# Performance work log

Measured on AMD Instinct MI355X. Metric: run time of the kernel, lower is better.

## Reference

```python
import jax, jax.numpy as jnp
import numpy as np

VOCAB = 2          # len(CHAR_VOCAB) in source
CE = 16            # char_embed_dim
CNN_OUT = 32 + 64 + 128  # 224
EMBED = 64


def _conv1d(x, w, b, pad):
    # x: [N, Cin, L]; w: [Cout, Cin, K]; torch Conv1d semantics
    y = jax.lax.conv_general_dilated(
        x, w, window_strides=(1,), padding=[(pad, pad)],
        dimension_numbers=('NCH', 'OIH', 'NCH'))
    return y + b[None, :, None]


def setup_inputs() -> dict:
    key = jax.random.key(0)
    ks = jax.random.split(key, 12)
    B, S, MC = 32, 2048, 20
    char_ids = jax.random.randint(ks[0], (B, S, MC), 0, VOCAB, dtype=jnp.int64)
    E = jax.random.normal(ks[1], (VOCAB, CE), jnp.float32)
    E = E.at[0].set(0.0)  # padding_idx=0
    s = 0.05
    return {
        'char_ids': char_ids,
        'E': E,
        'W1': jax.random.normal(ks[2], (32, CE, 1), jnp.float32) * s,
        'b1': jnp.zeros((32,), jnp.float32),
        'W2': jax.random.normal(ks[3], (64, CE, 2), jnp.float32) * s,
        'b2': jnp.zeros((64,), jnp.float32),
        'W3': jax.random.normal(ks[4], (128, CE, 3), jnp.float32) * s,
        'b3': jnp.zeros((128,), jnp.float32),
        'Ht_W': jax.random.normal(ks[5], (CNN_OUT, CNN_OUT), jnp.float32) * s,
        'Ht_b': jnp.zeros((CNN_OUT,), jnp.float32),
        'Hg_W': jax.random.normal(ks[6], (CNN_OUT, CNN_OUT), jnp.float32) * s,
        'Hg_b': jnp.zeros((CNN_OUT,), jnp.float32),
        'P_W': jax.random.normal(ks[7], (EMBED, CNN_OUT), jnp.float32) * s,
        'P_b': jnp.zeros((EMBED,), jnp.float32),
    }


def reference(char_ids, E, W1, b1, W2, b2, W3, b3, Ht_W, Ht_b, Hg_W, Hg_b, P_W, P_b):
    B, S, MC = char_ids.shape
    ids = char_ids.reshape(-1, MC)                      # [N, MC]
    emb = E[ids]                                        # [N, MC, CE]
    x = jnp.transpose(emb, (0, 2, 1))                   # [N, CE, MC]
    p1 = jnp.max(jax.nn.relu(_conv1d(x, W1, b1, 0)), axis=2)  # [N, 32]
    p2 = jnp.max(jax.nn.relu(_conv1d(x, W2, b2, 1)), axis=2)  # [N, 64]
    p3 = jnp.max(jax.nn.relu(_conv1d(x, W3, b3, 1)), axis=2)  # [N, 128]
    cnn = jnp.concatenate([p1, p2, p3], axis=1)         # [N, 224]
    t = jax.nn.relu(cnn @ Ht_W.T + Ht_b)
    g = jax.nn.sigmoid(cnn @ Hg_W.T + Hg_b)
    hw = g * t + (1.0 - g) * cnn
    out = hw @ P_W.T + P_b                              # [N, 64]
    return out.reshape(B, S, -1)
```

## Files before the change

### kernel.cpp

```cpp
#include <hip/hip_runtime.h>


typedef _Float16 f16;
typedef __attribute__((ext_vector_type(8))) _Float16 f16x8;
typedef __attribute__((ext_vector_type(4))) float f32x4;

#define LC1   0
#define LRAW2 96
#define LT2   672
#define LRAW3 1696
#define LT3LO 5152
#define LT3HI 7200
#define WOFFB    18944
#define PBASE    100352
#define NWTH     114688
#define UOUT_OFF 278528
#define NKEYS    4096
#define CROW     232
#define LUT_BLOCKS 45
#define REPACK_BLOCKS 448

__device__ __forceinline__ f16x8 hmax8(f16x8 a, f16x8 b) {
  return __builtin_elementwise_max(a, b);
}

__device__ __forceinline__ f16x8 pin8(f16x8 v) {
  union { f16x8 v; unsigned w[4]; } x; x.v = v;
  asm volatile("" : "+v"(x.w[0]), "+v"(x.w[1]), "+v"(x.w[2]), "+v"(x.w[3]) :: "memory");
  return x.v;
}

__device__ __forceinline__ float xs(const float* __restrict__ E, int s, int i) {
  return (s == 0) ? 0.f : E[(s - 1) * 16 + i];
}

__global__ __launch_bounds__(256) void prep_kernel(
    const float* __restrict__ E,
    const float* __restrict__ W1, const float* __restrict__ b1,
    const float* __restrict__ W2, const float* __restrict__ b2,
    const float* __restrict__ W3, const float* __restrict__ b3,
    const float* __restrict__ HtW, const float* __restrict__ HgW,
    const float* __restrict__ PW,
    f16* __restrict__ tab, f16* __restrict__ wsb)
{
  const int tid = threadIdx.x;
  const int bid = blockIdx.x;

  if (bid >= LUT_BLOCKS) {
    int idx = (bid - LUT_BLOCKS) * 256 + tid;
    if (idx < NWTH) {
      int e, isG = 0, isP = 0;
      if (idx < 50176)        { e = idx; }
      else if (idx < 100352)  { e = idx - 50176; isG = 1; }
      else                    { e = idx - 100352; isP = 1; }
      int col = e / 224, k = e - col * 224;
      int nf = col >> 4, kf = k >> 5, kr = k & 31;
      int lane = (col & 15) + ((kr >> 3) << 4), j = kr & 7;
      if (!isP) {
        int off = nf * 7168 + (isG * 7 + kf) * 512 + lane * 8 + j;
        wsb[off] = (f16)(isG ? HgW[e] : HtW[e]);
      } else {
        float w = PW[e];
        f16 hi = (f16)w;
        int off = PBASE + nf * 7168 + kf * 512 + lane * 8 + j;
        wsb[off] = hi;
        wsb[off + 3584] = (f16)(w - (float)hi);
      }
    }
    return;
  }

  if (bid < 27) {
    if (tid >= 128) return;
    const int c = tid, p = bid;
    const int sa = p / 9, sb = (p / 3) % 3, sc = p % 3;
    const float* w = W3 + c * 48;
    float acc = b3[c];
#pragma unroll
    for (int i = 0; i < 16; i++)
      acc += w[i * 3 + 0] * xs(E, sa, i) + w[i * 3 + 1] * xs(E, sb, i)
           + w[i * 3 + 2] * xs(E, sc, i);
    tab[LRAW3 + p * 128 + c] = (f16)acc;
    return;
  }
  if (bid < 43) {
    if (tid >= 128) return;
    const int c = tid, s = bid - 27;
    const float* w = W3 + c * 48;
    float lo = -65504.f, hi = -65504.f;
#pragma unroll
    for (int b = 0; b < 4; b++) {
      if (!((s >> b) & 1)) continue;
      int pl = 13 + 3 * (b >> 1) + (b & 1);
      int ph = 22 + 3 * (b >> 1) + (b & 1);
      int sal = pl / 9, sbl = (pl / 3) % 3, scl = pl % 3;
      int sah = ph / 9, sbh = (ph / 3) % 3, sch = ph % 3;
      float al = b3[c], ah = b3[c];
#pragma unroll
      for (int i = 0; i < 16; i++) {
        al += w[i * 3 + 0] * xs(E, sal, i) + w[i * 3 + 1] * xs(E, sbl, i)
            + w[i * 3 + 2] * xs(E, scl, i);
        ah += w[i * 3 + 0] * xs(E, sah, i) + w[i * 3 + 1] * xs(E, sbh, i)
            + w[i * 3 + 2] * xs(E, sch, i);
      }
      lo = fmaxf(lo, al);
      hi = fmaxf(hi, ah);
    }
    tab[LT3LO + s * 128 + c] = (f16)lo;
    tab[LT3HI + s * 128 + c] = (f16)hi;
    return;
  }
  if (bid == 43) {
    const int c = tid & 63, part = tid >> 6;
    const float* w = W2 + c * 32;
    if (part < 2) {
      int p0 = part * 5;
      int pend = part ? 9 : 5;
      for (int p = p0; p < pend; p++) {
        int sa = p / 3, sb = p % 3;
        float acc = b2[c];
#pragma unroll
        for (int i = 0; i < 16; i++)
          acc += w[i * 2 + 0] * xs(E, sa, i) + w[i * 2 + 1] * xs(E, sb, i);
        tab[LRAW2 + p * 64 + c] = (f16)acc;
      }
    } else {
      float u[4];
#pragma unroll
      for (int b = 0; b < 4; b++) {
        int p = 4 + 3 * (b >> 1) + (b & 1);
        int sa = p / 3, sb = p % 3;
        float acc = b2[c];
#pragma unroll
        for (int i = 0; i < 16; i++)
          acc += w[i * 2 + 0] * xs(E, sa, i) + w[i * 2 + 1] * xs(E, sb, i);
        u[b] = acc;
      }
      int s0 = (part - 2) * 8;
#pragma unroll
      for (int j = 0; j < 8; j++) {
        int s = s0 + j;
        float m = -65504.f;
#pragma unroll
        for (int b = 0; b < 4; b++)
          if ((s >> b) & 1) m = fmaxf(m, u[b]);
        tab[LT2 + s * 64 + c] = (f16)m;
      }
    }
    return;
  }
  {
    if (tid >= 32) return;
    const int c = tid;
    const float* w = W1 + c * 16;
    float u1 = b1[c], u2 = b1[c];
#pragma unroll
    for (int i = 0; i < 16; i++) {
      u1 += w[i] * E[i];
      u2 += w[i] * E[16 + i];
    }
    tab[LC1 + 0 * 32 + c] = (f16)fmaxf(u1, u2);
    tab[LC1 + 1 * 32 + c] = (f16)u1;
    tab[LC1 + 2 * 32 + c] = (f16)u2;
  }
}

__global__ __launch_bounds__(256) void ucompute_kernel(
    const f16* __restrict__ tab, const f16* __restrict__ wsb,
    const float* __restrict__ Htb, const float* __restrict__ Hgb,
    const float* __restrict__ Pb, float* __restrict__ uout)
{
  __shared__ __attribute__((aligned(16))) f16 cnn[16 * CROW];

  const int tid = threadIdx.x;
  const int wave = tid >> 6, lane = tid & 63;
  const int kbase = blockIdx.x * 16;
  const int lrow = lane & 15;
  const int kg8 = (lane >> 4) * 8;
  const int rr0 = (lane >> 4) * 4;

  const int p1row = tid >> 4;
  const int p1g = tid & 15;
  unsigned mw, mb;
  {
    unsigned key = (unsigned)(kbase + p1row);
    unsigned m3i = key & 255u;
    int st1 = 1 + (int)((key >> 8) & 1),  st2 = 1 + (int)((key >> 9) & 1);
    int st19 = 1 + (int)((key >> 10) & 1), st20 = 1 + (int)((key >> 11) & 1);
    unsigned m2i = 0, mchar = 0;
#pragma unroll
    for (int p = 0; p < 8; p++)
      if ((m3i >> p) & 1) {
        m2i |= (1u << (p >> 1)) | (1u << (p & 3));
        mchar |= (1u << ((p >> 2) & 1)) | (1u << ((p >> 1) & 1)) | (1u << (p & 1));
      }
    unsigned sel = (mchar == 3u) ? 0u : ((mchar & 1u) ? 1u : 2u);
    mw = m3i | (m2i << 8) | (sel << 12);
    mb = (unsigned)st1 | ((unsigned)(st20 * 3) << 4)
       | ((unsigned)(st1 * 3 + st2) << 8) | ((unsigned)(st19 * 9 + st20 * 3) << 16);
  }

  const f16x8 KZ = {0, 0, 0, 0, 0, 0, 0, 0};
  {
    const int m3 = mw & 255;
    f16x8 v = hmax8(*(const f16x8*)(tab + LT3LO + (m3 & 15) * 128 + p1g * 8),
                    *(const f16x8*)(tab + LT3HI + ((m3 >> 4) & 15) * 128 + p1g * 8));
    v = hmax8(v, *(const f16x8*)(tab + LRAW3 + ((mb >> 8) & 15) * 128 + p1g * 8));
    v = hmax8(v, *(const f16x8*)(tab + LRAW3 + ((mb >> 16) & 31) * 128 + p1g * 8));
    *(f16x8*)&cnn[p1row * CROW + 96 + p1g * 8] = hmax8(v, KZ);
    if (p1g < 8) {
      f16x8 u = *(const f16x8*)(tab + LT2 + ((mw >> 8) & 15) * 64 + p1g * 8);
      u = hmax8(u, *(const f16x8*)(tab + LRAW2 + (mb & 15) * 64 + p1g * 8));
      u = hmax8(u, *(const f16x8*)(tab + LRAW2 + ((mb >> 4) & 15) * 64 + p1g * 8));
      *(f16x8*)&cnn[p1row * CROW + 32 + p1g * 8] = hmax8(u, KZ);
    }
    if (p1g < 4) {
      int sel = (mw >> 12) & 3;
      f16x8 w = *(const f16x8*)(tab + LC1 + sel * 32 + p1g * 8);
      *(f16x8*)&cnn[p1row * CROW + p1g * 8] = hmax8(w, KZ);
    }
  }
  __syncthreads();

  f16x8 af[7];
#pragma unroll
  for (int kf = 0; kf < 7; kf++)
    af[kf] = *(const f16x8*)&cnn[lrow * CROW + kf * 32 + kg8];
#pragma unroll
  for (int kf = 0; kf < 7; kf++) af[kf] = pin8(af[kf]);
  __syncthreads();

  const f16* wbase = wsb + lane * 8;
  const int nf_cnt = (wave < 2) ? 4 : 3;
  for (int i = 0; i < nf_cnt; i++) {
    const int nf = wave + i * 4;
    const int col = nf * 16 + lrow;
    const f16* p_ = wbase + nf * 7168;
    const float bt = Htb[col], bg = Hgb[col];
    f32x4 aT = {bt, bt, bt, bt};
    f32x4 aG = {bg, bg, bg, bg};
#pragma unroll
    for (int kf = 0; kf < 7; kf++) {
      f16x8 wTv = *(const f16x8*)(p_ + kf * 512);
      f16x8 wGv = *(const f16x8*)(p_ + 3584 + kf * 512);
      aT = __builtin_amdgcn_mfma_f32_16x16x32_f16(af[kf], wTv, aT, 0, 0, 0);
      aG = __builtin_amdgcn_mfma_f32_16x16x32_f16(af[kf], wGv, aG, 0, 0, 0);
    }
#pragma unroll
    for (int r = 0; r < 4; r++) {
      int row = rr0 + r;
      float t  = fmaxf(aT[r], 0.f);
      float gg = __builtin_amdgcn_rcpf(1.f + __expf(-aG[r]));
      float cv = (float)cnn[row * CROW + col];
      cnn[row * CROW + col] = (f16)(cv + gg * (t - cv));
    }
  }
  __syncthreads();

  f16x8 ah[7];
#pragma unroll
  for (int kf = 0; kf < 7; kf++)
    ah[kf] = *(const f16x8*)&cnn[lrow * CROW + kf * 32 + kg8];
  {
    const int col = wave * 16 + lrow;
    const float bp = Pb[col];
    f32x4 ac = {bp, bp, bp, bp};
    const f16* ph = wbase + PBASE + wave * 7168;
#pragma unroll
    for (int kf = 0; kf < 7; kf++) {
      f16x8 wh = *(const f16x8*)(ph + kf * 512);
      f16x8 wl = *(const f16x8*)(ph + 3584 + kf * 512);
      ac = __builtin_amdgcn_mfma_f32_16x16x32_f16(ah[kf], wh, ac, 0, 0, 0);
      ac = __builtin_amdgcn_mfma_f32_16x16x32_f16(ah[kf], wl, ac, 0, 0, 0);
    }
#pragma unroll
    for (int r = 0; r < 4; r++)
      uout[(size_t)(kbase + rr0 + r) * 64 + col] = ac[r];
  }
}

__global__ __launch_bounds__(256) void keyscatter_kernel(
    const int* __restrict__ ids, const float* __restrict__ uout,
    float* __restrict__ out, int n_tok)
{
  __shared__ unsigned keys[64];
  const int tid = threadIdx.x;
  const int tok0 = blockIdx.x * 64;

  if (tid < 64) {
    unsigned key = 0;
    int t = tok0 + tid;
    if (t < n_tok) {
      const int4* idp4 = (const int4*)(ids + (size_t)t * 20);
      int st[21];
#pragma unroll
      for (int q = 0; q < 5; q++) {
        int4 v = idp4[q];
        st[q * 4 + 1] = v.x; st[q * 4 + 2] = v.y;
        st[q * 4 + 3] = v.z; st[q * 4 + 4] = v.w;
      }
      unsigned m3i = 0;
#pragma unroll
      for (int l = 1; l <= 18; l++)
        m3i |= 1u << ((st[l] << 2) | (st[l + 1] << 1) | st[l + 2]);
      key = m3i | ((unsigned)st[1] << 8) | ((unsigned)st[2] << 9)
          | ((unsigned)st[19] << 10) | ((unsigned)st[20] << 11);
    }
    keys[tid] = key;
  }
  __syncthreads();

  const int tl = tid >> 2, q = tid & 3;
  const int t = tok0 + tl;
  if (t >= n_tok) return;
  const f32x4* src = (const f32x4*)(uout + (size_t)keys[tl] * 64 + q * 16);
  f32x4 v0 = src[0], v1 = src[1], v2 = src[2], v3 = src[3];
  f32x4* dst = (f32x4*)(out + (size_t)t * 64 + q * 16);
  dst[0] = v0; dst[1] = v1; dst[2] = v2; dst[3] = v3;
}

extern "C" void kernel_launch(void* const* d_in, const int* in_sizes, int n_in,
                              void* d_out, int out_size, void* d_ws, size_t ws_size,
                              hipStream_t stream) {
  const int*   ids = (const int*)d_in[0];
  const float* E   = (const float*)d_in[1];
  const float* W1  = (const float*)d_in[2];
  const float* b1  = (const float*)d_in[3];
  const float* W2  = (const float*)d_in[4];
  const float* b2  = (const float*)d_in[5];
  const float* W3  = (const float*)d_in[6];
  const float* b3  = (const float*)d_in[7];
  const float* HtW = (const float*)d_in[8];
  const float* Htb = (const float*)d_in[9];
  const float* HgW = (const float*)d_in[10];
  const float* Hgb = (const float*)d_in[11];
  const float* PW  = (const float*)d_in[12];
  const float* Pb  = (const float*)d_in[13];
  float* out = (float*)d_out;
  char* ws = (char*)d_ws;
  f16* tab = (f16*)ws;
  f16* wsb = (f16*)(ws + WOFFB);
  float* uout = (float*)(ws + UOUT_OFF);
  const int n_tok = in_sizes[0] / 20;

  prep_kernel<<<LUT_BLOCKS + REPACK_BLOCKS, 256, 0, stream>>>(
      E, W1, b1, W2, b2, W3, b3, HtW, HgW, PW, tab, wsb);
  ucompute_kernel<<<NKEYS / 16, 256, 0, stream>>>(
      tab, wsb, Htb, Hgb, Pb, uout);
  keyscatter_kernel<<<(n_tok + 63) / 64, 256, 0, stream>>>(ids, uout, out, n_tok);
}
```

Baseline: 28.29 us.

## Move per-token key computation into prep kernel and widen scatter blocks

Per-token key hashing of the char ids moves out of the final scatter kernel into extra blocks of the prep kernel, so reading the large id array overlaps with weight repacking and LUT building instead of sitting on the critical path before the gather. The scatter kernel now reads precomputed 4-byte keys and handles 256 tokens per block across four segments, launching fewer blocks. This adds a workspace array of keys and an extra global write and read of those keys, and it makes the prep launch larger.

```diff
diff --git a/kernel.cpp b/kernel.cpp
--- a/kernel.cpp
+++ b/kernel.cpp
@@ -14,11 +14,13 @@
 #define WOFFB    18944
 #define PBASE    100352
 #define NWTH     114688
-#define UOUT_OFF 278528
+#define TKEY_OFF 278528
+#define UOUT_OFF 544768
 #define NKEYS    4096
 #define CROW     232
 #define LUT_BLOCKS 45
 #define REPACK_BLOCKS 448
+#define KEY_BLOCKS 256
 
 __device__ __forceinline__ f16x8 hmax8(f16x8 a, f16x8 b) {
   return __builtin_elementwise_max(a, b);
@@ -40,11 +42,32 @@
     const float* __restrict__ W2, const float* __restrict__ b2,
     const float* __restrict__ W3, const float* __restrict__ b3,
     const float* __restrict__ HtW, const float* __restrict__ HgW,
-    const float* __restrict__ PW,
-    f16* __restrict__ tab, f16* __restrict__ wsb)
+    const float* __restrict__ PW, const int* __restrict__ ids,
+    f16* __restrict__ tab, f16* __restrict__ wsb,
+    unsigned* __restrict__ tokkey, int n_tok)
 {
   const int tid = threadIdx.x;
   const int bid = blockIdx.x;
+
+  if (bid >= LUT_BLOCKS + REPACK_BLOCKS) {
+    int t = (bid - LUT_BLOCKS - REPACK_BLOCKS) * 256 + tid;
+    if (t >= n_tok) return;
+    const int4* idp4 = (const int4*)(ids + (size_t)t * 20);
+    int st[21];
+#pragma unroll
+    for (int q = 0; q < 5; q++) {
+      int4 v = idp4[q];
+      st[q * 4 + 1] = v.x; st[q * 4 + 2] = v.y;
+      st[q * 4 + 3] = v.z; st[q * 4 + 4] = v.w;
+    }
+    unsigned m3i = 0;
+#pragma unroll
+    for (int l = 1; l <= 18; l++)
+      m3i |= 1u << ((st[l] << 2) | (st[l + 1] << 1) | st[l + 2]);
+    tokkey[t] = m3i | ((unsigned)st[1] << 8) | ((unsigned)st[2] << 9)
+              | ((unsigned)st[19] << 10) | ((unsigned)st[20] << 11);
+    return;
+  }
 
   if (bid >= LUT_BLOCKS) {
     int idx = (bid - LUT_BLOCKS) * 256 + tid;
@@ -279,44 +302,31 @@
   }
 }
 
-__global__ __launch_bounds__(256) void keyscatter_kernel(
-    const int* __restrict__ ids, const float* __restrict__ uout,
+__global__ __launch_bounds__(256) void scatter_kernel(
+    const unsigned* __restrict__ tokkey, const float* __restrict__ uout,
     float* __restrict__ out, int n_tok)
 {
-  __shared__ unsigned keys[64];
+  __shared__ unsigned keys[256];
   const int tid = threadIdx.x;
-  const int tok0 = blockIdx.x * 64;
-
-  if (tid < 64) {
-    unsigned key = 0;
+  const int tok0 = blockIdx.x * 256;
+
+  {
     int t = tok0 + tid;
-    if (t < n_tok) {
-      const int4* idp4 = (const int4*)(ids + (size_t)t * 20);
-      int st[21];
-#pragma unroll
-      for (int q = 0; q < 5; q++) {
-        int4 v = idp4[q];
-        st[q * 4 + 1] = v.x; st[q * 4 + 2] = v.y;
-        st[q * 4 + 3] = v.z; st[q * 4 + 4] = v.w;
-      }
-      unsigned m3i = 0;
-#pragma unroll
-      for (int l = 1; l <= 18; l++)
-        m3i |= 1u << ((st[l] << 2) | (st[l + 1] << 1) | st[l + 2]);
-      key = m3i | ((unsigned)st[1] << 8) | ((unsigned)st[2] << 9)
-          | ((unsigned)st[19] << 10) | ((unsigned)st[20] << 11);
-    }
-    keys[tid] = key;
+    keys[tid] = (t < n_tok) ? tokkey[t] : 0u;
   }
   __syncthreads();
 
   const int tl = tid >> 2, q = tid & 3;
-  const int t = tok0 + tl;
-  if (t >= n_tok) return;
-  const f32x4* src = (const f32x4*)(uout + (size_t)keys[tl] * 64 + q * 16);
-  f32x4 v0 = src[0], v1 = src[1], v2 = src[2], v3 = src[3];
-  f32x4* dst = (f32x4*)(out + (size_t)t * 64 + q * 16);
-  dst[0] = v0; dst[1] = v1; dst[2] = v2; dst[3] = v3;
+#pragma unroll
+  for (int seg = 0; seg < 4; seg++) {
+    const int t = tok0 + seg * 64 + tl;
+    if (t >= n_tok) break;
+    const f32x4* src =
+        (const f32x4*)(uout + (size_t)keys[seg * 64 + tl] * 64 + q * 16);
+    f32x4 v0 = src[0], v1 = src[1], v2 = src[2], v3 = src[3];
+    f32x4* dst = (f32x4*)(out + (size_t)t * 64 + q * 16);
+    dst[0] = v0; dst[1] = v1; dst[2] = v2; dst[3] = v3;
+  }
 }
 
 extern "C" void kernel_launch(void* const* d_in, const int* in_sizes, int n_in,
@@ -340,12 +350,15 @@
   char* ws = (char*)d_ws;
   f16* tab = (f16*)ws;
   f16* wsb = (f16*)(ws + WOFFB);
+  unsigned* tokkey = (unsigned*)(ws + TKEY_OFF);
   float* uout = (float*)(ws + UOUT_OFF);
   const int n_tok = in_sizes[0] / 20;
 
-  prep_kernel<<<LUT_BLOCKS + REPACK_BLOCKS, 256, 0, stream>>>(
-      E, W1, b1, W2, b2, W3, b3, HtW, HgW, PW, tab, wsb);
+  const int key_blocks = (n_tok + 255) / 256;
+  prep_kernel<<<LUT_BLOCKS + REPACK_BLOCKS + key_blocks, 256, 0, stream>>>(
+      E, W1, b1, W2, b2, W3, b3, HtW, HgW, PW, ids, tab, wsb, tokkey, n_tok);
   ucompute_kernel<<<NKEYS / 16, 256, 0, stream>>>(
       tab, wsb, Htb, Hgb, Pb, uout);
-  keyscatter_kernel<<<(n_tok + 63) / 64, 256, 0, stream>>>(ids, uout, out, n_tok);
-}
+  scatter_kernel<<<(n_tok + 255) / 256, 256, 0, stream>>>(
+      tokkey, uout, out, n_tok);
+}
```

After: 27.50 us. -2.8%, faster.
